# Performance work log

Measured on AMD Instinct MI355X. Metric: run time of the kernel, lower is better.

Reference implementation:

```python
import jax, jax.numpy as jnp
import numpy as np

EMBED_DIM = 4096
NUM_Q_HEADS = 32
NUM_KV_HEADS = 8
HEAD_DIM = EMBED_DIM // NUM_Q_HEADS  # 128
GROUP = NUM_Q_HEADS // NUM_KV_HEADS  # 4
KV_SEQ_LEN = 1024
BATCH = 2
SEQ = 1024
THETA = 10000.0


def _rope(x, positions):
    # x: (B, T, H, D) with interleaved real/imag pairs along D (torch view_as_complex layout)
    half = x.shape[-1] // 2
    inv_freq = 1.0 / (THETA ** (jnp.arange(half, dtype=jnp.float32) / half))
    ang = positions[:, None].astype(jnp.float32) * inv_freq[None, :]  # (T, half)
    cos = jnp.cos(ang)[None, :, None, :].astype(x.dtype)
    sin = jnp.sin(ang)[None, :, None, :].astype(x.dtype)
    xr = x.reshape(*x.shape[:-1], half, 2)
    x0, x1 = xr[..., 0], xr[..., 1]
    o0 = x0 * cos - x1 * sin
    o1 = x0 * sin + x1 * cos
    return jnp.stack([o0, o1], axis=-1).reshape(x.shape)


def setup_inputs() -> dict:
    key = jax.random.key(0)
    ks = jax.random.split(key, 5)
    s_in = 1.0 / np.sqrt(EMBED_DIM)
    return {
        "x": jax.random.normal(ks[0], (BATCH, SEQ, EMBED_DIM), dtype=jnp.float32),
        "Wq": jax.random.normal(ks[1], (EMBED_DIM, EMBED_DIM), dtype=jnp.float32) * s_in,
        "Wk": jax.random.normal(ks[2], (NUM_KV_HEADS * HEAD_DIM, EMBED_DIM), dtype=jnp.float32) * s_in,
        "Wv": jax.random.normal(ks[3], (NUM_KV_HEADS * HEAD_DIM, EMBED_DIM), dtype=jnp.float32) * s_in,
        "Wo": jax.random.normal(ks[4], (EMBED_DIM, EMBED_DIM), dtype=jnp.float32) * s_in,
        "cache_k": jnp.zeros((BATCH, 2 * KV_SEQ_LEN, NUM_KV_HEADS, HEAD_DIM), dtype=jnp.float32),
        "cache_v": jnp.zeros((BATCH, 2 * KV_SEQ_LEN, NUM_KV_HEADS, HEAD_DIM), dtype=jnp.float32),
        "start_pos": 0,
    }


def reference(x, Wq, Wk, Wv, Wo, cache_k, cache_v, start_pos):
    B, T, C = x.shape
    end_pos = start_pos + T
    scale = 1.0 / np.sqrt(HEAD_DIM)

    q = (x @ Wq.T).reshape(B, T, NUM_Q_HEADS, HEAD_DIM)
    k = (x @ Wk.T).reshape(B, T, NUM_KV_HEADS, HEAD_DIM)
    v = (x @ Wv.T).reshape(B, T, NUM_KV_HEADS, HEAD_DIM)

    pos = start_pos + jnp.arange(T)
    q = _rope(q, pos)
    k = _rope(k, pos)

    # KV cache append (writes are detached in the original)
    cache_k = cache_k.at[:, start_pos:end_pos].set(jax.lax.stop_gradient(k))
    cache_v = cache_v.at[:, start_pos:end_pos].set(jax.lax.stop_gradient(v))
    k_full = cache_k[:, :end_pos]  # (B, S, Hkv, D)
    v_full = cache_v[:, :end_pos]

    # GQA without materializing repeated KV heads:
    # q head h attends kv head h // GROUP (matches repeat_interleave layout)
    q5 = q.transpose(0, 2, 1, 3).reshape(B, NUM_KV_HEADS, GROUP, T, HEAD_DIM)
    kh = k_full.transpose(0, 2, 1, 3)  # (B, Hkv, S, D)
    vh = v_full.transpose(0, 2, 1, 3)

    scores = jnp.einsum('bhgtd,bhsd->bhgts', q5, kh) * scale  # (B,Hkv,G,T,S)
    visible = jnp.arange(end_pos)[None, :] <= (start_pos + jnp.arange(T))[:, None]  # (T,S)
    scores = jnp.where(visible[None, None, None], scores, jnp.finfo(scores.dtype).min)
    probs = jax.nn.softmax(scores, axis=-1)
    ctx = jnp.einsum('bhgts,bhsd->bhgtd', probs, vh)

    out = ctx.reshape(B, NUM_Q_HEADS, T, HEAD_DIM).transpose(0, 2, 1, 3).reshape(B, T, C)
    return out @ Wo.T
```

## Files before the change

kernel.cpp:

```cpp
#include <hip/hip_runtime.h>
#include <stdint.h>

typedef unsigned short u16;
typedef __attribute__((ext_vector_type(8))) short short8x;
typedef __attribute__((ext_vector_type(4))) float floatx4;

#define TOKENS 2048
#define EMBED  4096
#define QKVN   6144
#define T_SEQ  1024
#define SMAX   2048
#define NQH    32
#define NKVH   8
#define HD     128

static __device__ __forceinline__ u16 f2b(float f) {
    union { float f; uint32_t u; } v; v.f = f;
    uint32_t r = v.u + 0x7fffu + ((v.u >> 16) & 1u);
    return (u16)(r >> 16);
}
static __device__ __forceinline__ float b2f(u16 h) {
    union { uint32_t u; float f; } v; v.u = ((uint32_t)h) << 16; return v.f;
}

static __device__ __forceinline__ void gload_lds16(const u16* g, u16* l) {
    __builtin_amdgcn_global_load_lds(
        (const __attribute__((address_space(1))) uint32_t*)g,
        (__attribute__((address_space(3))) uint32_t*)l, 16, 0, 0);
}

#define CSEG0 2097152
#define CSEG1 6291456
#define CSEG2 7340032
#define CSEG3 8388608
#define CSEG4 12582912
__global__ void convert_all_kernel(const float* __restrict__ x,  const float* __restrict__ Wq,
                                   const float* __restrict__ Wk, const float* __restrict__ Wv,
                                   const float* __restrict__ Wo,
                                   u16* __restrict__ xb, u16* __restrict__ wqkv,
                                   u16* __restrict__ wob) {
    int i = blockIdx.x * blockDim.x + threadIdx.x;
    if (i >= CSEG4) return;
    const float4* src; uint2* dst; int off;
    if (i < CSEG0)      { src = (const float4*)x;  dst = (uint2*)xb;   off = i; }
    else if (i < CSEG1) { src = (const float4*)Wq; dst = (uint2*)wqkv; off = i - CSEG0; }
    else if (i < CSEG2) { src = (const float4*)Wk; dst = (uint2*)wqkv + 4194304; off = i - CSEG1; }
    else if (i < CSEG3) { src = (const float4*)Wv; dst = (uint2*)wqkv + 5242880; off = i - CSEG2; }
    else                { src = (const float4*)Wo; dst = (uint2*)wob;  off = i - CSEG3; }
    float4 f = src[off];
    union { u16 h[4]; uint2 v; } o;
    o.h[0] = f2b(f.x); o.h[1] = f2b(f.y); o.h[2] = f2b(f.z); o.h[3] = f2b(f.w);
    dst[off] = o.v;
}

#define FENCE asm volatile("" ::: "memory")
#define WAIT5 asm volatile("s_waitcnt vmcnt(5)" ::: "memory")
#define WAIT0 asm volatile("s_waitcnt vmcnt(0)" ::: "memory")
#define NOSTG ((void)0)
#define NOLDB ((void)0)

#define HBA(BUF, H) (lds + (BUF) * 28672 + (H) * 8192)
#define HBB(BUF)    (lds + (BUF) * 28672 + 16384)
#define STGA(BUF, H, KT) do { \
    gload_lds16(gA[H][0] + (size_t)(KT) * 64, HBA(BUF, H) + dOffW); \
    gload_lds16(gA[H][1] + (size_t)(KT) * 64, HBA(BUF, H) + 4096 + dOffW); \
} while (0)
#define STGB(BUF, KT) do { \
    _Pragma("unroll") \
    for (int _L = 0; _L < 3; _L++) \
        gload_lds16(gBv[_L] + (size_t)(KT) * 64, HBB(BUF) + _L * 4096 + dOffW); \
} while (0)
#define LDAF(CBUF, AH) do { const u16* _p = HBA(CBUF, AH); \
    _Pragma("unroll") \
    for (int _mi = 0; _mi < 4; _mi++) { \
        af[_mi][0] = *(const short8x*)(_p + offA[_mi][0]); \
        af[_mi][1] = *(const short8x*)(_p + offA[_mi][1]); } } while (0)
#define LDBF(CBUF) do { const u16* _p = HBB(CBUF); \
    _Pragma("unroll") \
    for (int _nj = 0; _nj < 3; _nj++) { \
        bf[_nj][0] = *(const short8x*)(_p + offB[_nj][0]); \
        bf[_nj][1] = *(const short8x*)(_p + offB[_nj][1]); } } while (0)
#define PHASE(CBUF, AH, LOADB, STAGES, ENDW) do { \
    LDAF(CBUF, AH); \
    LOADB; \
    STAGES; \
    FENCE; __builtin_amdgcn_s_barrier(); FENCE; \
    __builtin_amdgcn_s_setprio(1); \
    _Pragma("unroll") \
    for (int _kk = 0; _kk < 2; _kk++) \
        _Pragma("unroll") \
        for (int _mi = 0; _mi < 4; _mi++) \
            _Pragma("unroll") \
            for (int _nj = 0; _nj < 3; _nj++) \
                acc[AH][_mi][_nj] = __builtin_amdgcn_mfma_f32_16x16x32_bf16( \
                    af[_mi][_kk], bf[_nj][_kk], acc[AH][_mi][_nj], 0, 0, 0); \
    __builtin_amdgcn_s_setprio(0); \
    ENDW; \
    FENCE; __builtin_amdgcn_s_barrier(); FENCE; \
} while (0)

__global__ __launch_bounds__(512, 1) void gemm256_kernel(
    const u16* __restrict__ A, const u16* __restrict__ Bw,
    u16* __restrict__ Cv, int N, int K) {
    extern __shared__ __align__(16) u16 lds[];
    const int tid = threadIdx.x;
    const int lane = tid & 63, w = tid >> 6;
    const int quad = lane >> 4, lc = lane & 15;
    const int wm = w >> 2, wn = w & 3;
    const int Mbase = blockIdx.y * 256, Nbase = blockIdx.x * 192;

    const int r8 = lane >> 3;
    const int sl = (lane & 7) ^ r8;
    const int srow = w * 8 + r8;
    const u16* gA[2][2];
    const u16* gBv[3];
#pragma unroll
    for (int H = 0; H < 2; H++)
#pragma unroll
        for (int L = 0; L < 2; L++)
            gA[H][L] = A + (size_t)(Mbase + H * 128 + L * 64 + srow) * K + sl * 8;
#pragma unroll
    for (int L = 0; L < 3; L++)
        gBv[L] = Bw + (size_t)(Nbase + L * 64 + srow) * K + sl * 8;
    const int dOffW = w * 512;

    int offA[4][2], offB[3][2];
    const int xsw = lc & 7;
#pragma unroll
    for (int mi = 0; mi < 4; mi++)
#pragma unroll
        for (int kk = 0; kk < 2; kk++)
            offA[mi][kk] = (wm * 64 + mi * 16 + lc) * 64 + (((kk * 4 + quad) ^ xsw) * 8);
#pragma unroll
    for (int nj = 0; nj < 3; nj++)
#pragma unroll
        for (int kk = 0; kk < 2; kk++)
            offB[nj][kk] = (wn * 48 + nj * 16 + lc) * 64 + (((kk * 4 + quad) ^ xsw) * 8);

    floatx4 acc[2][4][3] = {};
    short8x af[4][2];
    short8x bf[3][2];

    STGA(0, 0, 0); STGA(0, 1, 0); STGB(0, 0);
    STGA(1, 0, 1); STGB(1, 1);
    WAIT5;
    FENCE; __builtin_amdgcn_s_barrier(); FENCE;

    const int NT = K >> 6;
    for (int t = 0; t < NT - 2; t += 2) {
        PHASE(0, 0, LDBF(0), STGA(1, 1, t + 1), NOSTG);
        PHASE(0, 1, NOLDB, STGA(0, 0, t + 2); STGB(0, t + 2), WAIT5);
        PHASE(1, 0, LDBF(1), STGA(0, 1, t + 2), NOSTG);
        PHASE(1, 1, NOLDB, STGA(1, 0, t + 3); STGB(1, t + 3), WAIT5);
    }
    PHASE(0, 0, LDBF(0), STGA(1, 1, NT - 1), NOSTG);
    PHASE(0, 1, NOLDB, NOSTG, WAIT0);
    PHASE(1, 0, LDBF(1), NOSTG, NOSTG);
    PHASE(1, 1, NOLDB, NOSTG, NOSTG);

#pragma unroll
    for (int AH = 0; AH < 2; AH++)
#pragma unroll
        for (int mi = 0; mi < 4; mi++) {
            const int row0 = Mbase + AH * 128 + wm * 64 + mi * 16 + quad * 4;
#pragma unroll
            for (int nj = 0; nj < 3; nj++) {
                const int col = Nbase + wn * 48 + nj * 16 + lc;
#pragma unroll
                for (int r = 0; r < 4; r++)
                    Cv[(size_t)(row0 + r) * N + col] = f2b(acc[AH][mi][nj][r]);
            }
        }
}
#undef HBA
#undef HBB
#undef STGA
#undef STGB
#undef LDAF
#undef LDBF
#undef PHASE

#define HA2(BUF, H) (lds + (BUF) * 24576 + (H) * 4096)
#define HBB2(BUF)   (lds + (BUF) * 24576 + 8192)
#define STGA2(BUF, H, KT) gload_lds16(gA2[H] + (size_t)(KT) * 64, HA2(BUF, H) + dOffW)
#define STGB2(BUF, KT) do { \
    _Pragma("unroll") \
    for (int _L = 0; _L < 4; _L++) \
        gload_lds16(gB2[_L] + (size_t)(KT) * 64, HBB2(BUF) + _L * 4096 + dOffW); \
} while (0)
#define WAIT5K asm volatile("s_waitcnt vmcnt(5)" ::: "memory")
#define LDA2(CBUF, AH) do { const u16* _p = HA2(CBUF, AH); \
    _Pragma("unroll") \
    for (int _mi = 0; _mi < 2; _mi++) { \
        af2[_mi][0] = *(const short8x*)(_p + offA2[_mi][0]); \
        af2[_mi][1] = *(const short8x*)(_p + offA2[_mi][1]); } } while (0)
#define LDB2(CBUF) do { const u16* _p = HBB2(CBUF); \
    _Pragma("unroll") \
    for (int _nj = 0; _nj < 4; _nj++) { \
        bf2[_nj][0] = *(const short8x*)(_p + offB2[_nj][0]); \
        bf2[_nj][1] = *(const short8x*)(_p + offB2[_nj][1]); } } while (0)
#define PHASE2(CBUF, AH, LOADS, STAGES, ENDW) do { \
    LOADS; \
    STAGES; \
    FENCE; __builtin_amdgcn_s_barrier(); FENCE; \
    __builtin_amdgcn_s_setprio(1); \
    _Pragma("unroll") \
    for (int _kk = 0; _kk < 2; _kk++) \
        _Pragma("unroll") \
        for (int _mi = 0; _mi < 2; _mi++) \
            _Pragma("unroll") \
            for (int _nj = 0; _nj < 4; _nj++) \
                acc2[AH][_mi][_nj] = __builtin_amdgcn_mfma_f32_16x16x32_bf16( \
                    af2[_mi][_kk], bf2[_nj][_kk], acc2[AH][_mi][_nj], 0, 0, 0); \
    __builtin_amdgcn_s_setprio(0); \
    ENDW; \
    FENCE; __builtin_amdgcn_s_barrier(); FENCE; \
} while (0)

__global__ __launch_bounds__(512, 1) void gemmko_kernel(
    const u16* __restrict__ A, const u16* __restrict__ Bw,
    float* __restrict__ C, int N, int K) {
    extern __shared__ __align__(16) u16 lds[];
    const int tid = threadIdx.x;
    const int lane = tid & 63, w = tid >> 6;
    const int quad = lane >> 4, lc = lane & 15;
    const int wm = (w >> 2) & 1, wn = w & 3;
    const int Mbase = blockIdx.y * 128, Nbase = blockIdx.x * 256;

    const int r8 = lane >> 3;
    const int sl = (lane & 7) ^ r8;
    const int srow = w * 8 + r8;
    const u16* gA2[2];
    const u16* gB2[4];
#pragma unroll
    for (int H = 0; H < 2; H++)
        gA2[H] = A + (size_t)(Mbase + H * 64 + srow) * K + sl * 8;
#pragma unroll
    for (int L = 0; L < 4; L++)
        gB2[L] = Bw + (size_t)(Nbase + L * 64 + srow) * K + sl * 8;
    const int dOffW = w * 512;

    int offA2[2][2], offB2[4][2];
    const int xsw = lc & 7;
#pragma unroll
    for (int mi = 0; mi < 2; mi++)
#pragma unroll
        for (int kk = 0; kk < 2; kk++)
            offA2[mi][kk] = (wm * 32 + mi * 16 + lc) * 64 + (((kk * 4 + quad) ^ xsw) * 8);
#pragma unroll
    for (int nj = 0; nj < 4; nj++)
#pragma unroll
        for (int kk = 0; kk < 2; kk++)
            offB2[nj][kk] = (wn * 64 + nj * 16 + lc) * 64 + (((kk * 4 + quad) ^ xsw) * 8);

    floatx4 acc2[2][2][4] = {};
    short8x af2[2][2], bf2[4][2];

    STGA2(0, 0, 0); STGA2(0, 1, 0); STGB2(0, 0);
    STGA2(1, 0, 1); STGB2(1, 1);
    WAIT5K;
    FENCE; __builtin_amdgcn_s_barrier(); FENCE;

    const int NT = K >> 6;
    for (int t = 0; t < NT - 2; t += 2) {
        PHASE2(0, 0, LDA2(0, 0); LDB2(0), STGA2(1, 1, t + 1), NOSTG);
        PHASE2(0, 1, LDA2(0, 1), STGA2(0, 0, t + 2); STGB2(0, t + 2), WAIT5K);
        PHASE2(1, 0, LDA2(1, 0); LDB2(1), STGA2(0, 1, t + 2), NOSTG);
        PHASE2(1, 1, LDA2(1, 1), STGA2(1, 0, t + 3); STGB2(1, t + 3), WAIT5K);
    }
    PHASE2(0, 0, LDA2(0, 0); LDB2(0), STGA2(1, 1, NT - 1), NOSTG);
    PHASE2(0, 1, LDA2(0, 1), NOSTG, WAIT0);
    PHASE2(1, 0, LDA2(1, 0); LDB2(1), NOSTG, NOSTG);
    PHASE2(1, 1, LDA2(1, 1), NOSTG, NOSTG);

#pragma unroll
    for (int AH = 0; AH < 2; AH++)
#pragma unroll
        for (int mi = 0; mi < 2; mi++) {
            const int row0 = Mbase + AH * 64 + wm * 32 + mi * 16 + quad * 4;
#pragma unroll
            for (int nj = 0; nj < 4; nj++) {
                const int col = Nbase + wn * 64 + nj * 16 + lc;
#pragma unroll
                for (int r = 0; r < 4; r++)
                    C[(size_t)(row0 + r) * N + col] = acc2[AH][mi][nj][r];
            }
        }
}
#undef HA2
#undef HBB2
#undef STGA2
#undef STGB2
#undef WAIT5K
#undef LDA2
#undef LDB2
#undef PHASE2
#undef WAIT5
#undef WAIT0
#undef NOSTG
#undef NOLDB
#undef FENCE

__global__ void cache_prefix_kernel(const float* __restrict__ ck, const float* __restrict__ cv,
                                    const int* __restrict__ sp,
                                    u16* __restrict__ kh, u16* __restrict__ vt8) {
    int spos = sp[0];
    long total = (long)2 * spos * NKVH * HD;
    for (long i = (long)blockIdx.x * blockDim.x + threadIdx.x; i < total; i += (long)gridDim.x * blockDim.x) {
        long d = i % HD, rest = i / HD;
        long g = rest % NKVH; rest /= NKVH;
        long s = rest % spos; long b = rest / spos;
        float kv = ck[((b * SMAX + s) * NKVH + g) * HD + d];
        kh[((b * NKVH + g) * SMAX + s) * HD + d] = f2b(kv);
        float vv = cv[((b * SMAX + s) * NKVH + g) * HD + d];
        vt8[(size_t)(b * NKVH + g) * SMAX * HD + (s >> 3) * 1024 + d * 8 + (s & 7)] = f2b(vv);
    }
}

__global__ void rope_qk_kernel(const u16* __restrict__ qkvb, const int* __restrict__ sp,
                               u16* __restrict__ qh, u16* __restrict__ kh) {
    int spos = sp[0];
    int idx = blockIdx.x * blockDim.x + threadIdx.x;
    int tok = idx / 2560;
    int u = idx - tok * 2560;
    int b = tok >> 10, t = tok & 1023;
    float pos = (float)(spos + t);
    const u16* src = qkvb + (size_t)tok * QKVN;
    const float kScale = 0.08838834764831845f;
    const float kLog = -0.20762050593045857f;
    if (u < 2048) {
        int h = u >> 6, i = u & 63;
        float ang = pos * exp2f((float)i * kLog);
        float cs = cosf(ang), sn = sinf(ang);
        float x0 = b2f(src[h * HD + 2 * i]), x1 = b2f(src[h * HD + 2 * i + 1]);
        size_t dst = (((size_t)(b * NQH + h) * T_SEQ) + t) * HD + 2 * i;
        qh[dst]     = f2b((x0 * cs - x1 * sn) * kScale);
        qh[dst + 1] = f2b((x0 * sn + x1 * cs) * kScale);
    } else {
        int u2 = u - 2048;
        int g = u2 >> 6, i = u2 & 63;
        float ang = pos * exp2f((float)i * kLog);
        float cs = cosf(ang), sn = sinf(ang);
        float x0 = b2f(src[EMBED + g * HD + 2 * i]), x1 = b2f(src[EMBED + g * HD + 2 * i + 1]);
        size_t dst = (((size_t)(b * NKVH + g) * SMAX) + spos + t) * HD + 2 * i;
        kh[dst]     = f2b(x0 * cs - x1 * sn);
        kh[dst + 1] = f2b(x0 * sn + x1 * cs);
    }
}

__global__ __launch_bounds__(256) void vpack_kernel(const u16* __restrict__ qkvb,
                                                    const int* __restrict__ sp,
                                                    u16* __restrict__ vt8) {
    __shared__ u16 lds[16 * 136];
    int spos = sp[0];
    int tile = blockIdx.x;
    int t16 = tile & 63;
    int g = (tile >> 6) & 7;
    int b = tile >> 9;
    int tok0 = t16 * 16;
    int tid = threadIdx.x;
    {
        int srow = tid >> 4, dc8 = (tid & 15) * 8;
        const u16* src = qkvb + (size_t)(b * T_SEQ + tok0 + srow) * QKVN + 5120 + g * HD + dc8;
        *(uint4*)(lds + srow * 136 + dc8) = *(const uint4*)src;
    }
    __syncthreads();
    int d = tid & 127, half = tid >> 7;
    u16* vpg = vt8 + (size_t)(b * NKVH + g) * SMAX * HD;
    int s0 = spos + tok0;
    u16 val[8];
#pragma unroll
    for (int k = 0; k < 8; k++) val[k] = lds[(half * 8 + k) * 136 + d];
    if ((s0 & 7) == 0) {
        union { u16 h[8]; uint4 u; } pk;
#pragma unroll
        for (int k = 0; k < 8; k++) pk.h[k] = val[k];
        *(uint4*)(vpg + (size_t)((s0 >> 3) + half) * 1024 + d * 8) = pk.u;
    } else {
#pragma unroll
        for (int k = 0; k < 8; k++) {
            int s = s0 + half * 8 + k;
            vpg[(size_t)(s >> 3) * 1024 + d * 8 + (s & 7)] = val[k];
        }
    }
}

__global__ __launch_bounds__(256, 2) void attn_kernel(
    const u16* __restrict__ qh, const u16* __restrict__ kh,
    const u16* __restrict__ vt8, const int* __restrict__ sp,
    u16* __restrict__ ctx) {
    extern __shared__ __align__(16) char smem[];
    int spos = sp[0];
    int tid = threadIdx.x, w = tid >> 6, lane = tid & 63;
    int quad = lane >> 4, lc = lane & 15;
    int tile = blockIdx.x;
    int j = 63 - (tile & 63);
    int g = (tile >> 6) & 7;
    int b = tile >> 9;
    int qbase = j * 16;

    const u16* kp = kh + (size_t)(b * NKVH + g) * SMAX * HD;
    const u16* vp = vt8 + (size_t)(b * NKVH + g) * SMAX * HD;

    short8x qf[4][4];
#pragma unroll
    for (int m = 0; m < 4; m++) {
        const u16* qp = qh + ((size_t)(b * NQH + g * 4 + m) * T_SEQ + qbase + lc) * HD + quad * 8;
#pragma unroll
        for (int dc = 0; dc < 4; dc++)
            qf[m][dc] = *(const short8x*)(qp + dc * 32);
    }
    short8x ones;
#pragma unroll
    for (int jj = 0; jj < 8; jj++) ones[jj] = (short)0x3F80;

    floatx4 o[4][8] = {};
    floatx4 lacc[4] = {};
    int rowpos = spos + qbase + quad * 4;
    int nch = (spos + qbase + 16 + 63) >> 6;
    u16* pw = (u16*)smem + w * 4608;

    for (int c = w; c < nch; c += 4) {
        int koff = c * 64;
#pragma unroll
        for (int st = 0; st < 4; st++) {
            const u16* kr = kp + (size_t)(koff + st * 16 + lc) * HD + quad * 8;
            floatx4 sc[4] = {};
#pragma unroll
            for (int dc = 0; dc < 4; dc++) {
                short8x kf = *(const short8x*)(kr + dc * 32);
#pragma unroll
                for (int m = 0; m < 4; m++)
                    sc[m] = __builtin_amdgcn_mfma_f32_16x16x32_bf16(qf[m][dc], kf, sc[m], 0, 0, 0);
            }
            int skey = koff + st * 16 + lc;
#pragma unroll
            for (int m = 0; m < 4; m++)
#pragma unroll
                for (int r = 0; r < 4; r++) {
                    float p = (skey <= rowpos + r) ? __expf(sc[m][r]) : 0.0f;
                    pw[m * 1152 + (quad * 4 + r) * 72 + st * 16 + lc] = f2b(p);
                }
        }
        asm volatile("s_waitcnt lgkmcnt(0)" ::: "memory");
#pragma unroll
        for (int hf = 0; hf < 2; hf++) {
            short8x pf[4];
#pragma unroll
            for (int m = 0; m < 4; m++)
                pf[m] = *(const short8x*)(pw + m * 1152 + lc * 72 + hf * 32 + quad * 8);
#pragma unroll
            for (int m = 0; m < 4; m++)
                lacc[m] = __builtin_amdgcn_mfma_f32_16x16x32_bf16(pf[m], ones, lacc[m], 0, 0, 0);
            const u16* vbase = vp + ((size_t)koff << 7) + (size_t)(hf * 4 + quad) * 1024 + lc * 8;
#pragma unroll
            for (int dc8 = 0; dc8 < 8; dc8++) {
                short8x vf = *(const short8x*)(vbase + dc8 * 128);
#pragma unroll
                for (int m = 0; m < 4; m++)
                    o[m][dc8] = __builtin_amdgcn_mfma_f32_16x16x32_bf16(pf[m], vf, o[m][dc8], 0, 0, 0);
            }
        }
    }

    float* obuf = (float*)smem;
    float* lbuf = (float*)(smem + 33792);
    for (int ph = 0; ph < 4; ph++) {
        __syncthreads();
        if (w == ph) {
            if (ph == 0) {
#pragma unroll
                for (int m = 0; m < 4; m++) {
#pragma unroll
                    for (int dc8 = 0; dc8 < 8; dc8++)
#pragma unroll
                        for (int r = 0; r < 4; r++)
                            obuf[(m * 16 + quad * 4 + r) * 132 + dc8 * 16 + lc] = o[m][dc8][r];
#pragma unroll
                    for (int r = 0; r < 4; r++) lbuf[m * 16 + quad * 4 + r] = lacc[m][r];
                }
            } else {
#pragma unroll
                for (int m = 0; m < 4; m++) {
#pragma unroll
                    for (int dc8 = 0; dc8 < 8; dc8++)
#pragma unroll
                        for (int r = 0; r < 4; r++)
                            obuf[(m * 16 + quad * 4 + r) * 132 + dc8 * 16 + lc] += o[m][dc8][r];
#pragma unroll
                    for (int r = 0; r < 4; r++) lbuf[m * 16 + quad * 4 + r] += lacc[m][r];
                }
            }
        }
    }
    __syncthreads();

    int row = tid >> 2;
    int m = row >> 4;
    int cb = (tid & 3) * 32;
    float inv = 1.0f / lbuf[row];
    int token = qbase + (row & 15);
    size_t base = ((size_t)(b * T_SEQ + token) * NQH + g * 4 + m) * HD + cb;
#pragma unroll
    for (int v4 = 0; v4 < 4; v4++) {
        union { u16 h[8]; uint4 u; } pk;
#pragma unroll
        for (int jj = 0; jj < 8; jj++)
            pk.h[jj] = f2b(obuf[row * 132 + cb + v4 * 8 + jj] * inv);
        *(uint4*)(ctx + base + v4 * 8) = pk.u;
    }
}

extern "C" void kernel_launch(void* const* d_in, const int* in_sizes, int n_in,
                              void* d_out, int out_size, void* d_ws, size_t ws_size,
                              hipStream_t stream) {
    const float* x  = (const float*)d_in[0];
    const float* Wq = (const float*)d_in[1];
    const float* Wk = (const float*)d_in[2];
    const float* Wv = (const float*)d_in[3];
    const float* Wo = (const float*)d_in[4];
    const float* ck = (const float*)d_in[5];
    const float* cv = (const float*)d_in[6];
    const int*   sp = (const int*)d_in[7];

    char* p = (char*)d_ws;
    u16* xb   = (u16*)p;
    u16* qh   = xb;
    p += (size_t)TOKENS * EMBED * 2;
    u16* wqkv = (u16*)p; p += (size_t)QKVN * EMBED * 2;
    u16* wob  = (u16*)p; p += (size_t)EMBED * EMBED * 2;
    u16* qkvb = (u16*)p;
    u16* ctx  = qkvb;
    p += (size_t)TOKENS * QKVN * 2;
    u16* kh   = (u16*)p; p += (size_t)2 * NKVH * SMAX * HD * 2;
    u16* vt8  = (u16*)p;

    static int gemm_attr = 0;
    if (!gemm_attr) {
        (void)hipFuncSetAttribute(reinterpret_cast<const void*>(&gemm256_kernel),
                                  hipFuncAttributeMaxDynamicSharedMemorySize, 114688);
        (void)hipFuncSetAttribute(reinterpret_cast<const void*>(&gemmko_kernel),
                                  hipFuncAttributeMaxDynamicSharedMemorySize, 98304);
        gemm_attr = 1;
    }

    convert_all_kernel<<<(CSEG4 + 255) / 256, 256, 0, stream>>>(x, Wq, Wk, Wv, Wo, xb, wqkv, wob);
    gemm256_kernel<<<dim3(QKVN / 192, TOKENS / 256), 512, 114688, stream>>>(xb, wqkv, qkvb, QKVN, EMBED);
    cache_prefix_kernel<<<256, 256, 0, stream>>>(ck, cv, sp, kh, vt8);
    rope_qk_kernel<<<TOKENS * 2560 / 256, 256, 0, stream>>>(qkvb, sp, qh, kh);
    vpack_kernel<<<1024, 256, 0, stream>>>(qkvb, sp, vt8);
    attn_kernel<<<1024, 256, 36864, stream>>>(qh, kh, vt8, sp, ctx);
    gemmko_kernel<<<dim3(EMBED / 256, TOKENS / 128), 512, 98304, stream>>>(ctx, wob, (float*)d_out, EMBED, EMBED);
}
```

Before: 322.1 us.

## Restructure GEMM main loops into single-barrier full-tile phases with simple double buffering

Both bf16 GEMM kernels (QKV projection and output projection) drop the four-phase half-tile ping-pong schedule. Each k-step now loads both A halves and B from one LDS buffer, issues the whole next k-tile of global-to-LDS loads, and runs all MFMAs in a single phase with one barrier. The vmcnt(5) partial waits become a full vmcnt(0) wait at the end of each phase, and a sched_barrier keeps the second A-fragment reads after the load issue. This halves the barriers per k-tile and simplifies the schedule. In exchange, each phase now waits for the whole next tile to land, so less load latency is hidden behind compute, and register pressure is higher.

```diff
diff --git a/kernel.cpp b/kernel.cpp
--- a/kernel.cpp
+++ b/kernel.cpp
@@ -54,10 +54,9 @@
 }
 
 #define FENCE asm volatile("" ::: "memory")
-#define WAIT5 asm volatile("s_waitcnt vmcnt(5)" ::: "memory")
-#define WAIT0 asm volatile("s_waitcnt vmcnt(0)" ::: "memory")
+#define WAITZ asm volatile("s_waitcnt vmcnt(0)" ::: "memory")
 #define NOSTG ((void)0)
-#define NOLDB ((void)0)
+#define NOW   ((void)0)
 
 #define HBA(BUF, H) (lds + (BUF) * 28672 + (H) * 8192)
 #define HBB(BUF)    (lds + (BUF) * 28672 + 16384)
@@ -70,21 +69,26 @@
     for (int _L = 0; _L < 3; _L++) \
         gload_lds16(gBv[_L] + (size_t)(KT) * 64, HBB(BUF) + _L * 4096 + dOffW); \
 } while (0)
-#define LDAF(CBUF, AH) do { const u16* _p = HBA(CBUF, AH); \
+#define STGALL(BUF, KT) do { STGA(BUF, 0, KT); STGA(BUF, 1, KT); STGB(BUF, KT); } while (0)
+#define PH1(CBUF, STAGES, ENDW) do { \
+    const u16* _pa0 = HBA(CBUF, 0); \
+    const u16* _pa1 = HBA(CBUF, 1); \
+    const u16* _pb  = HBB(CBUF); \
+    short8x af0[4][2], af1[4][2], bf[3][2]; \
     _Pragma("unroll") \
     for (int _mi = 0; _mi < 4; _mi++) { \
-        af[_mi][0] = *(const short8x*)(_p + offA[_mi][0]); \
-        af[_mi][1] = *(const short8x*)(_p + offA[_mi][1]); } } while (0)
-#define LDBF(CBUF) do { const u16* _p = HBB(CBUF); \
+        af0[_mi][0] = *(const short8x*)(_pa0 + offA[_mi][0]); \
+        af0[_mi][1] = *(const short8x*)(_pa0 + offA[_mi][1]); } \
     _Pragma("unroll") \
     for (int _nj = 0; _nj < 3; _nj++) { \
-        bf[_nj][0] = *(const short8x*)(_p + offB[_nj][0]); \
-        bf[_nj][1] = *(const short8x*)(_p + offB[_nj][1]); } } while (0)
-#define PHASE(CBUF, AH, LOADB, STAGES, ENDW) do { \
-    LDAF(CBUF, AH); \
-    LOADB; \
+        bf[_nj][0] = *(const short8x*)(_pb + offB[_nj][0]); \
+        bf[_nj][1] = *(const short8x*)(_pb + offB[_nj][1]); } \
     STAGES; \
-    FENCE; __builtin_amdgcn_s_barrier(); FENCE; \
+    __builtin_amdgcn_sched_barrier(0); \
+    _Pragma("unroll") \
+    for (int _mi = 0; _mi < 4; _mi++) { \
+        af1[_mi][0] = *(const short8x*)(_pa1 + offA[_mi][0]); \
+        af1[_mi][1] = *(const short8x*)(_pa1 + offA[_mi][1]); } \
     __builtin_amdgcn_s_setprio(1); \
     _Pragma("unroll") \
     for (int _kk = 0; _kk < 2; _kk++) \
@@ -92,8 +96,16 @@
         for (int _mi = 0; _mi < 4; _mi++) \
             _Pragma("unroll") \
             for (int _nj = 0; _nj < 3; _nj++) \
-                acc[AH][_mi][_nj] = __builtin_amdgcn_mfma_f32_16x16x32_bf16( \
-                    af[_mi][_kk], bf[_nj][_kk], acc[AH][_mi][_nj], 0, 0, 0); \
+                acc[0][_mi][_nj] = __builtin_amdgcn_mfma_f32_16x16x32_bf16( \
+                    af0[_mi][_kk], bf[_nj][_kk], acc[0][_mi][_nj], 0, 0, 0); \
+    _Pragma("unroll") \
+    for (int _kk = 0; _kk < 2; _kk++) \
+        _Pragma("unroll") \
+        for (int _mi = 0; _mi < 4; _mi++) \
+            _Pragma("unroll") \
+            for (int _nj = 0; _nj < 3; _nj++) \
+                acc[1][_mi][_nj] = __builtin_amdgcn_mfma_f32_16x16x32_bf16( \
+                    af1[_mi][_kk], bf[_nj][_kk], acc[1][_mi][_nj], 0, 0, 0); \
     __builtin_amdgcn_s_setprio(0); \
     ENDW; \
     FENCE; __builtin_amdgcn_s_barrier(); FENCE; \
@@ -138,25 +150,18 @@
             offB[nj][kk] = (wn * 48 + nj * 16 + lc) * 64 + (((kk * 4 + quad) ^ xsw) * 8);
 
     floatx4 acc[2][4][3] = {};
-    short8x af[4][2];
-    short8x bf[3][2];
-
-    STGA(0, 0, 0); STGA(0, 1, 0); STGB(0, 0);
-    STGA(1, 0, 1); STGB(1, 1);
-    WAIT5;
+
+    STGALL(0, 0);
+    WAITZ;
     FENCE; __builtin_amdgcn_s_barrier(); FENCE;
 
     const int NT = K >> 6;
     for (int t = 0; t < NT - 2; t += 2) {
-        PHASE(0, 0, LDBF(0), STGA(1, 1, t + 1), NOSTG);
-        PHASE(0, 1, NOLDB, STGA(0, 0, t + 2); STGB(0, t + 2), WAIT5);
-        PHASE(1, 0, LDBF(1), STGA(0, 1, t + 2), NOSTG);
-        PHASE(1, 1, NOLDB, STGA(1, 0, t + 3); STGB(1, t + 3), WAIT5);
-    }
-    PHASE(0, 0, LDBF(0), STGA(1, 1, NT - 1), NOSTG);
-    PHASE(0, 1, NOLDB, NOSTG, WAIT0);
-    PHASE(1, 0, LDBF(1), NOSTG, NOSTG);
-    PHASE(1, 1, NOLDB, NOSTG, NOSTG);
+        PH1(0, STGALL(1, t + 1), WAITZ);
+        PH1(1, STGALL(0, t + 2), WAITZ);
+    }
+    PH1(0, STGALL(1, NT - 1), WAITZ);
+    PH1(1, NOSTG, NOW);
 
 #pragma unroll
     for (int AH = 0; AH < 2; AH++)
@@ -176,9 +181,8 @@
 #undef HBB
 #undef STGA
 #undef STGB
-#undef LDAF
-#undef LDBF
-#undef PHASE
+#undef STGALL
+#undef PH1
 
 #define HA2(BUF, H) (lds + (BUF) * 24576 + (H) * 4096)
 #define HBB2(BUF)   (lds + (BUF) * 24576 + 8192)
@@ -188,21 +192,26 @@
     for (int _L = 0; _L < 4; _L++) \
         gload_lds16(gB2[_L] + (size_t)(KT) * 64, HBB2(BUF) + _L * 4096 + dOffW); \
 } while (0)
-#define WAIT5K asm volatile("s_waitcnt vmcnt(5)" ::: "memory")
-#define LDA2(CBUF, AH) do { const u16* _p = HA2(CBUF, AH); \
+#define STGALL2(BUF, KT) do { STGA2(BUF, 0, KT); STGA2(BUF, 1, KT); STGB2(BUF, KT); } while (0)
+#define PH2(CBUF, STAGES, ENDW) do { \
+    const u16* _pa0 = HA2(CBUF, 0); \
+    const u16* _pa1 = HA2(CBUF, 1); \
+    const u16* _pb  = HBB2(CBUF); \
+    short8x af0[2][2], af1[2][2], bf2[4][2]; \
     _Pragma("unroll") \
     for (int _mi = 0; _mi < 2; _mi++) { \
-        af2[_mi][0] = *(const short8x*)(_p + offA2[_mi][0]); \
-        af2[_mi][1] = *(const short8x*)(_p + offA2[_mi][1]); } } while (0)
-#define LDB2(CBUF) do { const u16* _p = HBB2(CBUF); \
+        af0[_mi][0] = *(const short8x*)(_pa0 + offA2[_mi][0]); \
+        af0[_mi][1] = *(const short8x*)(_pa0 + offA2[_mi][1]); } \
     _Pragma("unroll") \
     for (int _nj = 0; _nj < 4; _nj++) { \
-        bf2[_nj][0] = *(const short8x*)(_p + offB2[_nj][0]); \
-        bf2[_nj][1] = *(const short8x*)(_p + offB2[_nj][1]); } } while (0)
-#define PHASE2(CBUF, AH, LOADS, STAGES, ENDW) do { \
-    LOADS; \
+        bf2[_nj][0] = *(const short8x*)(_pb + offB2[_nj][0]); \
+        bf2[_nj][1] = *(const short8x*)(_pb + offB2[_nj][1]); } \
     STAGES; \
-    FENCE; __builtin_amdgcn_s_barrier(); FENCE; \
+    __builtin_amdgcn_sched_barrier(0); \
+    _Pragma("unroll") \
+    for (int _mi = 0; _mi < 2; _mi++) { \
+        af1[_mi][0] = *(const short8x*)(_pa1 + offA2[_mi][0]); \
+        af1[_mi][1] = *(const short8x*)(_pa1 + offA2[_mi][1]); } \
     __builtin_amdgcn_s_setprio(1); \
     _Pragma("unroll") \
     for (int _kk = 0; _kk < 2; _kk++) \
@@ -210,8 +219,16 @@
         for (int _mi = 0; _mi < 2; _mi++) \
             _Pragma("unroll") \
             for (int _nj = 0; _nj < 4; _nj++) \
-                acc2[AH][_mi][_nj] = __builtin_amdgcn_mfma_f32_16x16x32_bf16( \
-                    af2[_mi][_kk], bf2[_nj][_kk], acc2[AH][_mi][_nj], 0, 0, 0); \
+                acc2[0][_mi][_nj] = __builtin_amdgcn_mfma_f32_16x16x32_bf16( \
+                    af0[_mi][_kk], bf2[_nj][_kk], acc2[0][_mi][_nj], 0, 0, 0); \
+    _Pragma("unroll") \
+    for (int _kk = 0; _kk < 2; _kk++) \
+        _Pragma("unroll") \
+        for (int _mi = 0; _mi < 2; _mi++) \
+            _Pragma("unroll") \
+            for (int _nj = 0; _nj < 4; _nj++) \
+                acc2[1][_mi][_nj] = __builtin_amdgcn_mfma_f32_16x16x32_bf16( \
+                    af1[_mi][_kk], bf2[_nj][_kk], acc2[1][_mi][_nj], 0, 0, 0); \
     __builtin_amdgcn_s_setprio(0); \
     ENDW; \
     FENCE; __builtin_amdgcn_s_barrier(); FENCE; \
@@ -254,24 +271,18 @@
             offB2[nj][kk] = (wn * 64 + nj * 16 + lc) * 64 + (((kk * 4 + quad) ^ xsw) * 8);
 
     floatx4 acc2[2][2][4] = {};
-    short8x af2[2][2], bf2[4][2];
-
-    STGA2(0, 0, 0); STGA2(0, 1, 0); STGB2(0, 0);
-    STGA2(1, 0, 1); STGB2(1, 1);
-    WAIT5K;
+
+    STGALL2(0, 0);
+    WAITZ;
     FENCE; __builtin_amdgcn_s_barrier(); FENCE;
 
     const int NT = K >> 6;
     for (int t = 0; t < NT - 2; t += 2) {
-        PHASE2(0, 0, LDA2(0, 0); LDB2(0), STGA2(1, 1, t + 1), NOSTG);
-        PHASE2(0, 1, LDA2(0, 1), STGA2(0, 0, t + 2); STGB2(0, t + 2), WAIT5K);
-        PHASE2(1, 0, LDA2(1, 0); LDB2(1), STGA2(0, 1, t + 2), NOSTG);
-        PHASE2(1, 1, LDA2(1, 1), STGA2(1, 0, t + 3); STGB2(1, t + 3), WAIT5K);
-    }
-    PHASE2(0, 0, LDA2(0, 0); LDB2(0), STGA2(1, 1, NT - 1), NOSTG);
-    PHASE2(0, 1, LDA2(0, 1), NOSTG, WAIT0);
-    PHASE2(1, 0, LDA2(1, 0); LDB2(1), NOSTG, NOSTG);
-    PHASE2(1, 1, LDA2(1, 1), NOSTG, NOSTG);
+        PH2(0, STGALL2(1, t + 1), WAITZ);
+        PH2(1, STGALL2(0, t + 2), WAITZ);
+    }
+    PH2(0, STGALL2(1, NT - 1), WAITZ);
+    PH2(1, NOSTG, NOW);
 
 #pragma unroll
     for (int AH = 0; AH < 2; AH++)
@@ -291,14 +302,11 @@
 #undef HBB2
 #undef STGA2
 #undef STGB2
-#undef WAIT5K
-#undef LDA2
-#undef LDB2
-#undef PHASE2
-#undef WAIT5
-#undef WAIT0
+#undef STGALL2
+#undef PH2
+#undef WAITZ
 #undef NOSTG
-#undef NOLDB
+#undef NOW
 #undef FENCE
 
 __global__ void cache_prefix_kernel(const float* __restrict__ ck, const float* __restrict__ cv,
```

Result: faster. 314.8 us (median of 2 runs) (-2.3%).
